# Kernel optimization log

Hardware: AMD Instinct MI355X
Metric: run time of the kernel (lower is better)

Reference implementation:

```python
import jax, jax.numpy as jnp
import numpy as np

EPS = 1e-08  # matches torch default eps in both F.normalize and PairwiseDistance


def setup_inputs() -> dict:
    key = jax.random.key(0)
    x = jax.random.normal(key, (8192, 1024), dtype=jnp.float32)
    return {"x": x}


def reference(x) -> jnp.ndarray:
    B = x.shape[0]
    # F.normalize(x, p=2, dim=-1, eps=EPS): x / max(||x||_2, eps)
    norms = jnp.linalg.norm(x, axis=-1, keepdims=True)
    xn = x / jnp.maximum(norms, EPS)
    # cosine similarity matrix [B, B]
    cos_sim = xn @ xn.T
    # fill_diagonal_(-2): exclude self from nearest-neighbor search
    idx = jnp.arange(B)
    cos_sim = cos_sim.at[idx, idx].set(-2.0)
    nn_idx = jnp.argmax(cos_sim, axis=1)  # [B] int
    # torch PairwiseDistance(p=2, eps=EPS): ||x1 - x2 + eps||_2
    diff = xn - xn[nn_idx] + EPS
    nn_dist = jnp.sqrt(jnp.sum(diff * diff, axis=-1))  # [B]
    loss = -jnp.mean(jnp.log(nn_dist + EPS))
    return loss
```

## Files before the change

kernel.cpp:

```cpp
#include <hip/hip_runtime.h>
#include <hip/hip_bf16.h>
#include <math.h>

#define NB 8192
#define ND 1024
#define KEPS 1e-8f
#define SLOTS 128
#define NTILE 32
#define NWG 528
#define NKT 16

typedef __attribute__((ext_vector_type(8))) __bf16 bf16x8;
typedef __attribute__((ext_vector_type(4))) float f32x4;

__device__ __forceinline__ unsigned int fmono(float f) {
    unsigned int b = __float_as_uint(f);
    return b ^ ((b & 0x80000000u) ? 0xFFFFFFFFu : 0x80000000u);
}
__device__ __forceinline__ unsigned short f2bf(float f) {
    union { float f; unsigned int u; } a;
    a.f = f;
    unsigned int lsb = (a.u >> 16) & 1u;
    a.u += 0x7fffu + lsb;
    return (unsigned short)(a.u >> 16);
}
__device__ __forceinline__ void gload_lds16(const void* g, void* l) {
    __builtin_amdgcn_global_load_lds(
        (const __attribute__((address_space(1))) unsigned int*)g,
        (__attribute__((address_space(3))) unsigned int*)l, 16, 0, 0);
}
__device__ __forceinline__ unsigned long long packmax(float mx, int mc) {
    return ((unsigned long long)fmono(mx) << 32) |
           (unsigned long long)(~(unsigned int)mc);
}

__global__ __launch_bounds__(256) void normalize_k(const float* __restrict__ x,
                                                   unsigned short* __restrict__ xnb) {
    int row = blockIdx.x * 4 + (threadIdx.x >> 6);
    int l = threadIdx.x & 63;
    const float4* xr = (const float4*)(x + (size_t)row * ND);
    float4 v[4];
    float ss = 0.f;
#pragma unroll
    for (int q = 0; q < 4; ++q) {
        v[q] = xr[q * 64 + l];
        ss += v[q].x * v[q].x + v[q].y * v[q].y + v[q].z * v[q].z + v[q].w * v[q].w;
    }
#pragma unroll
    for (int off = 1; off < 64; off <<= 1) ss += __shfl_xor(ss, off, 64);
    float scale = 1.0f / fmaxf(sqrtf(ss), KEPS);
    ushort4* o = (ushort4*)(xnb + (size_t)row * ND);
#pragma unroll
    for (int q = 0; q < 4; ++q) {
        ushort4 u;
        u.x = f2bf(v[q].x * scale);
        u.y = f2bf(v[q].y * scale);
        u.z = f2bf(v[q].z * scale);
        u.w = f2bf(v[q].w * scale);
        o[q * 64 + l] = u;
    }
}

#define FENCE_BARRIER() do { asm volatile("" ::: "memory"); \
    __builtin_amdgcn_s_barrier(); asm volatile("" ::: "memory"); } while (0)
#define LGKM0() do { asm volatile("s_waitcnt lgkmcnt(0)" ::: "memory"); \
    __builtin_amdgcn_sched_barrier(0); } while (0)
#define WAIT_VM6() asm volatile("s_waitcnt vmcnt(6)" ::: "memory")
#define WAIT_VM0() asm volatile("s_waitcnt vmcnt(0)" ::: "memory")

#define STAGE(H, DB) do { \
    gload_lds16(sp[H][0], ldsb + (DB) + (H) * 16384 + wv * 1024); \
    gload_lds16(sp[H][1], ldsb + (DB) + (H) * 16384 + 8192 + wv * 1024); \
    sp[H][0] += 128; sp[H][1] += 128; } while (0)

#define LOAD_A(CB, MQ) do { \
    const char* Ab_ = ldsb + (CB) + ((MQ) * 2 + wM) * 8192 + rowOff; \
    _Pragma("unroll") for (int mi = 0; mi < 4; ++mi) { \
        af[mi][0] = *(const bf16x8*)(Ab_ + mi * 2048 + ks0); \
        af[mi][1] = *(const bf16x8*)(Ab_ + mi * 2048 + ks1); } } while (0)

#define LOAD_B(CB, BANK, NQ) do { \
    const char* Bb_ = ldsb + (CB) + 32768 + (NQ) * 16384 + wN * 4096 + rowOff; \
    _Pragma("unroll") for (int ni = 0; ni < 2; ++ni) { \
        BANK[ni][0] = *(const bf16x8*)(Bb_ + ni * 2048 + ks0); \
        BANK[ni][1] = *(const bf16x8*)(Bb_ + ni * 2048 + ks1); } } while (0)

#define MFMAQ(MH, NH, BANK) do { \
    __builtin_amdgcn_s_setprio(1); \
    _Pragma("unroll") for (int mi = 0; mi < 4; ++mi) \
    _Pragma("unroll") for (int ni = 0; ni < 2; ++ni) { \
        acc[(MH) * 4 + mi][(NH) * 2 + ni] = __builtin_amdgcn_mfma_f32_16x16x32_bf16( \
            af[mi][0], BANK[ni][0], acc[(MH) * 4 + mi][(NH) * 2 + ni], 0, 0, 0); \
        acc[(MH) * 4 + mi][(NH) * 2 + ni] = __builtin_amdgcn_mfma_f32_16x16x32_bf16( \
            af[mi][1], BANK[ni][1], acc[(MH) * 4 + mi][(NH) * 2 + ni], 0, 0, 0); } \
    __builtin_amdgcn_s_setprio(0); } while (0)

#define KTILE(CB, DB, S1, S2, FINAL) do { \
    bf16x8 af[4][2], b0[2][2], b1[2][2]; \
    LOAD_A(CB, 0); LOAD_B(CB, b0, 0); \
    if (S1) STAGE(1, DB); \
    FENCE_BARRIER(); LGKM0(); MFMAQ(0, 0, b0); FENCE_BARRIER(); \
    LOAD_B(CB, b1, 1); \
    if (S2) STAGE(0, CB); \
    FENCE_BARRIER(); LGKM0(); MFMAQ(0, 1, b1); FENCE_BARRIER(); \
    LOAD_A(CB, 1); \
    if (S2) STAGE(2, CB); \
    FENCE_BARRIER(); LGKM0(); MFMAQ(1, 1, b1); FENCE_BARRIER(); \
    if (S2) STAGE(3, CB); \
    FENCE_BARRIER(); MFMAQ(1, 0, b0); \
    if (FINAL) { WAIT_VM0(); } else { WAIT_VM6(); } \
    FENCE_BARRIER(); } while (0)

#define KTILE_LAST(CB) do { \
    bf16x8 af[4][2], b0[2][2], b1[2][2]; \
    LOAD_A(CB, 0); LOAD_B(CB, b0, 0); \
    FENCE_BARRIER(); LGKM0(); MFMAQ(0, 0, b0); FENCE_BARRIER(); \
    LOAD_B(CB, b1, 1); \
    FENCE_BARRIER(); LGKM0(); MFMAQ(0, 1, b1); FENCE_BARRIER(); \
    LOAD_A(CB, 1); \
    FENCE_BARRIER(); LGKM0(); MFMAQ(1, 1, b1); FENCE_BARRIER(); \
    MFMAQ(1, 0, b0); } while (0)

__global__ __launch_bounds__(512, 2) void argmax_gemm(const unsigned short* __restrict__ xnb,
                                                      unsigned long long* __restrict__ partial) {
    extern __shared__ char ldsb[];

    int wg = (int)blockIdx.x;
    int tile = (wg & 7) * (NWG / 8) + (wg >> 3);
    int by = 0, tr = tile;
    while (tr >= NTILE - by) { tr -= NTILE - by; ++by; }
    const int bx = by + tr;

    const int rowBase = by * 256, colBase = bx * 256;
    const int tid = (int)threadIdx.x;
    const int wv = tid >> 6;
    const int l = tid & 63;
    const int wM = wv >> 2;
    const int wN = wv & 3;

    const int rowOff = (l & 15) * 128;
    const int ks0 = (((l >> 4) * 16)) ^ ((l & 7) << 4);
    const int ks1 = (64 | ((l >> 4) * 16)) ^ ((l & 7) << 4);

    const int scol = (((l & 7) ^ (l >> 3)) << 4);
    const char* xb = (const char*)xnb;
    const char* sp[4][2];
#pragma unroll
    for (int q = 0; q < 2; ++q) {
        int R = (q * 8 + wv) * 8 + (l >> 3);
        int arow = (R >> 6) * 128 + (R & 63);
        int bcol = (R >> 5) * 64 + (R & 31);
        sp[0][q] = xb + (size_t)(rowBase + arow) * 2048 + scol;
        sp[1][q] = xb + (size_t)(rowBase + arow + 64) * 2048 + scol;
        sp[2][q] = xb + (size_t)(colBase + bcol) * 2048 + scol;
        sp[3][q] = xb + (size_t)(colBase + bcol + 32) * 2048 + scol;
    }

    f32x4 acc[8][4];
#pragma unroll
    for (int m = 0; m < 8; ++m)
#pragma unroll
        for (int n = 0; n < 4; ++n) acc[m][n] = f32x4{0.f, 0.f, 0.f, 0.f};

    STAGE(0, 0); STAGE(2, 0); STAGE(3, 0); STAGE(1, 0);
    STAGE(0, 65536); STAGE(2, 65536); STAGE(3, 65536);
    WAIT_VM6();
    FENCE_BARRIER();

    for (int c = 0; c < 12; c += 2) {
        KTILE(0, 65536, true, true, false);
        KTILE(65536, 0, true, true, false);
    }
    KTILE(0, 65536, true, true, false);
    KTILE(65536, 0, true, true, false);
    KTILE(0, 65536, true, false, true);
    KTILE_LAST(65536);

#pragma unroll
    for (int m = 0; m < 8; ++m) {
#pragma unroll
        for (int r = 0; r < 4; ++r) {
            int gi = rowBase + wM * 128 + m * 16 + (l >> 4) * 4 + r;
            float mx = -3.0f;
            int mc = 0x7FFFFFFF;
#pragma unroll
            for (int n = 0; n < 4; ++n) {
                int gj = colBase + wN * 64 + n * 16 + (l & 15);
                float v = (gi == gj) ? -2.0f : acc[m][n][r];
                if (v > mx) { mx = v; mc = gj; }
            }
#pragma unroll
            for (int off = 1; off < 16; off <<= 1) {
                float omx = __shfl_xor(mx, off, 64);
                int omc = __shfl_xor(mc, off, 64);
                if (omx > mx || (omx == mx && omc < mc)) { mx = omx; mc = omc; }
            }
            if ((l & 15) == 0)
                partial[(size_t)gi * SLOTS + (2 * by + (bx - by) * 4 + wN)] = packmax(mx, mc);
        }
    }
    if (bx > by) {
#pragma unroll
        for (int n = 0; n < 4; ++n) {
            int gj = colBase + wN * 64 + n * 16 + (l & 15);
            float mx = -3.0f;
            int mc = 0x7FFFFFFF;
#pragma unroll
            for (int m = 0; m < 8; ++m) {
#pragma unroll
                for (int r = 0; r < 4; ++r) {
                    int gi = rowBase + wM * 128 + m * 16 + (l >> 4) * 4 + r;
                    float v = (gi == gj) ? -2.0f : acc[m][n][r];
                    if (v > mx) { mx = v; mc = gi; }
                }
            }
#pragma unroll
            for (int off = 16; off < 64; off <<= 1) {
                float omx = __shfl_xor(mx, off, 64);
                int omc = __shfl_xor(mc, off, 64);
                if (omx > mx || (omx == mx && omc < mc)) { mx = omx; mc = omc; }
            }
            if ((l >> 4) == 0)
                partial[(size_t)gj * SLOTS + (2 * by + wM)] = packmax(mx, mc);
        }
    }
}

__global__ __launch_bounds__(256) void dist_k(const float* __restrict__ x,
                                              const unsigned long long* __restrict__ partial,
                                              float* __restrict__ rowloss) {
    int i = blockIdx.x * 4 + (threadIdx.x >> 6);
    int l = threadIdx.x & 63;
    int nv = SLOTS - 2 * (i >> 8);
    unsigned long long p = 0ull;
    if (l < nv) p = partial[(size_t)i * SLOTS + l];
    if (l + 64 < nv) {
        unsigned long long o = partial[(size_t)i * SLOTS + l + 64];
        if (o > p) p = o;
    }
#pragma unroll
    for (int off = 1; off < 64; off <<= 1) {
        unsigned long long o = __shfl_xor(p, off, 64);
        if (o > p) p = o;
    }
    int j = (int)(~(unsigned int)(p & 0xFFFFFFFFull));

    const float4* xi = (const float4*)(x + (size_t)i * ND);
    const float4* xj = (const float4*)(x + (size_t)j * ND);
    float4 a[4], b[4];
    float sa = 0.f, sb = 0.f;
#pragma unroll
    for (int q = 0; q < 4; ++q) {
        a[q] = xi[q * 64 + l];
        b[q] = xj[q * 64 + l];
        sa += a[q].x * a[q].x + a[q].y * a[q].y + a[q].z * a[q].z + a[q].w * a[q].w;
        sb += b[q].x * b[q].x + b[q].y * b[q].y + b[q].z * b[q].z + b[q].w * b[q].w;
    }
#pragma unroll
    for (int off = 1; off < 64; off <<= 1) {
        sa += __shfl_xor(sa, off, 64);
        sb += __shfl_xor(sb, off, 64);
    }
    float ia = 1.0f / fmaxf(sqrtf(sa), KEPS);
    float ib = 1.0f / fmaxf(sqrtf(sb), KEPS);
    float ss = 0.f;
#pragma unroll
    for (int q = 0; q < 4; ++q) {
        float dx = a[q].x * ia - b[q].x * ib + KEPS;
        float dy = a[q].y * ia - b[q].y * ib + KEPS;
        float dz = a[q].z * ia - b[q].z * ib + KEPS;
        float dw = a[q].w * ia - b[q].w * ib + KEPS;
        ss += dx * dx + dy * dy + dz * dz + dw * dw;
    }
#pragma unroll
    for (int off = 1; off < 64; off <<= 1) ss += __shfl_xor(ss, off, 64);
    if (l == 0) rowloss[i] = -logf(sqrtf(ss) + KEPS);
}

__global__ __launch_bounds__(1024) void reduce_k(const float* __restrict__ rowloss,
                                                 float* __restrict__ out) {
    int t = threadIdx.x;
    float s = 0.0f;
#pragma unroll
    for (int k = 0; k < 8; ++k) s += rowloss[t + k * 1024];
#pragma unroll
    for (int off = 32; off > 0; off >>= 1) s += __shfl_down(s, off, 64);
    __shared__ float sred[16];
    if ((t & 63) == 0) sred[t >> 6] = s;
    __syncthreads();
    if (t == 0) {
        float tot = 0.0f;
        for (int k = 0; k < 16; ++k) tot += sred[k];
        out[0] = tot / (float)NB;
    }
}

extern "C" void kernel_launch(void* const* d_in, const int* in_sizes, int n_in,
                              void* d_out, int out_size, void* d_ws, size_t ws_size,
                              hipStream_t stream) {
    const float* x = (const float*)d_in[0];
    float* out = (float*)d_out;

    char* ws = (char*)d_ws;
    unsigned short* xnb = (unsigned short*)ws;
    unsigned long long* partial =
        (unsigned long long*)(ws + (size_t)NB * ND * 2);
    float* rowloss = (float*)(ws + (size_t)NB * ND * 2 + (size_t)NB * SLOTS * 8);

    (void)hipFuncSetAttribute((const void*)argmax_gemm,
                              hipFuncAttributeMaxDynamicSharedMemorySize, 131072);

    normalize_k<<<NB / 4, 256, 0, stream>>>(x, xnb);
    argmax_gemm<<<NWG, 512, 131072, stream>>>(xnb, partial);
    dist_k<<<NB / 4, 256, 0, stream>>>(x, partial, rowloss);
    reduce_k<<<1, 1024, 0, stream>>>(rowloss, out);
}
```

Measured before the change: 217.6 us.

## Simplify GEMM K-loop to whole-tile prefetch and fuse final reduction into dist kernel

Replaces the interleaved, fine-grained staging schedule in the GEMM main loop with a simple double-buffer. Each k-tile now issues all four global-to-LDS stages for the next buffer up front, then waits and runs all MFMAs, without intermediate barriers, lgkm waits or setprio. Separately, the reduce kernel is removed: the last dist_k block, found via an atomic counter reset in normalize_k, sums the row losses, saving one launch. The simpler schedule may lose the overlap that the fine-grained interleaving gave.

```diff
diff --git a/kernel.cpp b/kernel.cpp
--- a/kernel.cpp
+++ b/kernel.cpp
@@ -9,6 +9,7 @@
 #define NTILE 32
 #define NWG 528
 #define NKT 16
+#define NDBLK (NB / 4)
 
 typedef __attribute__((ext_vector_type(8))) __bf16 bf16x8;
 typedef __attribute__((ext_vector_type(4))) float f32x4;
@@ -35,7 +36,9 @@
 }
 
 __global__ __launch_bounds__(256) void normalize_k(const float* __restrict__ x,
-                                                   unsigned short* __restrict__ xnb) {
+                                                   unsigned short* __restrict__ xnb,
+                                                   unsigned int* __restrict__ counter) {
+    if (blockIdx.x == 0 && threadIdx.x == 0) counter[0] = 0u;
     int row = blockIdx.x * 4 + (threadIdx.x >> 6);
     int l = threadIdx.x & 63;
     const float4* xr = (const float4*)(x + (size_t)row * ND);
@@ -63,9 +66,7 @@
 
 #define FENCE_BARRIER() do { asm volatile("" ::: "memory"); \
     __builtin_amdgcn_s_barrier(); asm volatile("" ::: "memory"); } while (0)
-#define LGKM0() do { asm volatile("s_waitcnt lgkmcnt(0)" ::: "memory"); \
-    __builtin_amdgcn_sched_barrier(0); } while (0)
-#define WAIT_VM6() asm volatile("s_waitcnt vmcnt(6)" ::: "memory")
+#define WAIT_VM8() asm volatile("s_waitcnt vmcnt(8)" ::: "memory")
 #define WAIT_VM0() asm volatile("s_waitcnt vmcnt(0)" ::: "memory")
 
 #define STAGE(H, DB) do { \
@@ -86,40 +87,23 @@
         BANK[ni][1] = *(const bf16x8*)(Bb_ + ni * 2048 + ks1); } } while (0)
 
 #define MFMAQ(MH, NH, BANK) do { \
-    __builtin_amdgcn_s_setprio(1); \
     _Pragma("unroll") for (int mi = 0; mi < 4; ++mi) \
     _Pragma("unroll") for (int ni = 0; ni < 2; ++ni) { \
         acc[(MH) * 4 + mi][(NH) * 2 + ni] = __builtin_amdgcn_mfma_f32_16x16x32_bf16( \
             af[mi][0], BANK[ni][0], acc[(MH) * 4 + mi][(NH) * 2 + ni], 0, 0, 0); \
         acc[(MH) * 4 + mi][(NH) * 2 + ni] = __builtin_amdgcn_mfma_f32_16x16x32_bf16( \
             af[mi][1], BANK[ni][1], acc[(MH) * 4 + mi][(NH) * 2 + ni], 0, 0, 0); } \
-    __builtin_amdgcn_s_setprio(0); } while (0)
-
-#define KTILE(CB, DB, S1, S2, FINAL) do { \
+    } while (0)
+
+#define KT(CB, DB, PF) do { \
+    if (PF) { STAGE(0, DB); STAGE(1, DB); STAGE(2, DB); STAGE(3, DB); WAIT_VM8(); } \
+    else { WAIT_VM0(); } \
+    FENCE_BARRIER(); \
     bf16x8 af[4][2], b0[2][2], b1[2][2]; \
-    LOAD_A(CB, 0); LOAD_B(CB, b0, 0); \
-    if (S1) STAGE(1, DB); \
-    FENCE_BARRIER(); LGKM0(); MFMAQ(0, 0, b0); FENCE_BARRIER(); \
-    LOAD_B(CB, b1, 1); \
-    if (S2) STAGE(0, CB); \
-    FENCE_BARRIER(); LGKM0(); MFMAQ(0, 1, b1); FENCE_BARRIER(); \
-    LOAD_A(CB, 1); \
-    if (S2) STAGE(2, CB); \
-    FENCE_BARRIER(); LGKM0(); MFMAQ(1, 1, b1); FENCE_BARRIER(); \
-    if (S2) STAGE(3, CB); \
-    FENCE_BARRIER(); MFMAQ(1, 0, b0); \
-    if (FINAL) { WAIT_VM0(); } else { WAIT_VM6(); } \
+    LOAD_A(CB, 0); LOAD_B(CB, b0, 0); MFMAQ(0, 0, b0); \
+    LOAD_B(CB, b1, 1); MFMAQ(0, 1, b1); \
+    LOAD_A(CB, 1); MFMAQ(1, 1, b1); MFMAQ(1, 0, b0); \
     FENCE_BARRIER(); } while (0)
-
-#define KTILE_LAST(CB) do { \
-    bf16x8 af[4][2], b0[2][2], b1[2][2]; \
-    LOAD_A(CB, 0); LOAD_B(CB, b0, 0); \
-    FENCE_BARRIER(); LGKM0(); MFMAQ(0, 0, b0); FENCE_BARRIER(); \
-    LOAD_B(CB, b1, 1); \
-    FENCE_BARRIER(); LGKM0(); MFMAQ(0, 1, b1); FENCE_BARRIER(); \
-    LOAD_A(CB, 1); \
-    FENCE_BARRIER(); LGKM0(); MFMAQ(1, 1, b1); FENCE_BARRIER(); \
-    MFMAQ(1, 0, b0); } while (0)
 
 __global__ __launch_bounds__(512, 2) void argmax_gemm(const unsigned short* __restrict__ xnb,
                                                       unsigned long long* __restrict__ partial) {
@@ -156,25 +140,18 @@
         sp[3][q] = xb + (size_t)(colBase + bcol + 32) * 2048 + scol;
     }
 
+    STAGE(0, 0); STAGE(1, 0); STAGE(2, 0); STAGE(3, 0);
+
     f32x4 acc[8][4];
 #pragma unroll
     for (int m = 0; m < 8; ++m)
 #pragma unroll
         for (int n = 0; n < 4; ++n) acc[m][n] = f32x4{0.f, 0.f, 0.f, 0.f};
 
-    STAGE(0, 0); STAGE(2, 0); STAGE(3, 0); STAGE(1, 0);
-    STAGE(0, 65536); STAGE(2, 65536); STAGE(3, 65536);
-    WAIT_VM6();
-    FENCE_BARRIER();
-
-    for (int c = 0; c < 12; c += 2) {
-        KTILE(0, 65536, true, true, false);
-        KTILE(65536, 0, true, true, false);
-    }
-    KTILE(0, 65536, true, true, false);
-    KTILE(65536, 0, true, true, false);
-    KTILE(0, 65536, true, false, true);
-    KTILE_LAST(65536);
+    for (int c = 0; c < NKT; c += 2) {
+        KT(0, 65536, c + 1 < NKT);
+        KT(65536, 0, c + 2 < NKT);
+    }
 
 #pragma unroll
     for (int m = 0; m < 8; ++m) {
@@ -228,7 +205,9 @@
 
 __global__ __launch_bounds__(256) void dist_k(const float* __restrict__ x,
                                               const unsigned long long* __restrict__ partial,
-                                              float* __restrict__ rowloss) {
+                                              float* __restrict__ rowloss,
+                                              unsigned int* __restrict__ counter,
+                                              float* __restrict__ out) {
     int i = blockIdx.x * 4 + (threadIdx.x >> 6);
     int l = threadIdx.x & 63;
     int nv = SLOTS - 2 * (i >> 8);
@@ -274,24 +253,29 @@
     }
 #pragma unroll
     for (int off = 1; off < 64; off <<= 1) ss += __shfl_xor(ss, off, 64);
-    if (l == 0) rowloss[i] = -logf(sqrtf(ss) + KEPS);
-}
-
-__global__ __launch_bounds__(1024) void reduce_k(const float* __restrict__ rowloss,
-                                                 float* __restrict__ out) {
-    int t = threadIdx.x;
-    float s = 0.0f;
-#pragma unroll
-    for (int k = 0; k < 8; ++k) s += rowloss[t + k * 1024];
-#pragma unroll
-    for (int off = 32; off > 0; off >>= 1) s += __shfl_down(s, off, 64);
-    __shared__ float sred[16];
-    if ((t & 63) == 0) sred[t >> 6] = s;
+    if (l == 0) rowloss[i] = logf(sqrtf(ss) + KEPS);
+
+    __shared__ int done_s;
     __syncthreads();
-    if (t == 0) {
-        float tot = 0.0f;
-        for (int k = 0; k < 16; ++k) tot += sred[k];
-        out[0] = tot / (float)NB;
+    if (threadIdx.x == 0) {
+        __threadfence();
+        unsigned int old = atomicAdd(counter, 1u);
+        done_s = (old == (unsigned int)(NDBLK - 1)) ? 1 : 0;
+    }
+    __syncthreads();
+    if (done_s) {
+        __threadfence();
+        int t = threadIdx.x;
+        float s = 0.f;
+#pragma unroll
+        for (int k = 0; k < 32; ++k) s += rowloss[t * 32 + k];
+#pragma unroll
+        for (int off = 1; off < 64; off <<= 1) s += __shfl_xor(s, off, 64);
+        __shared__ float fred[4];
+        if ((t & 63) == 0) fred[t >> 6] = s;
+        __syncthreads();
+        if (t == 0)
+            out[0] = -(fred[0] + fred[1] + fred[2] + fred[3]) / (float)NB;
     }
 }
 
@@ -306,12 +290,12 @@
     unsigned long long* partial =
         (unsigned long long*)(ws + (size_t)NB * ND * 2);
     float* rowloss = (float*)(ws + (size_t)NB * ND * 2 + (size_t)NB * SLOTS * 8);
+    unsigned int* counter = (unsigned int*)(rowloss + NB);
 
     (void)hipFuncSetAttribute((const void*)argmax_gemm,
                               hipFuncAttributeMaxDynamicSharedMemorySize, 131072);
 
-    normalize_k<<<NB / 4, 256, 0, stream>>>(x, xnb);
+    normalize_k<<<NB / 4, 256, 0, stream>>>(x, xnb, counter);
     argmax_gemm<<<NWG, 512, 131072, stream>>>(xnb, partial);
-    dist_k<<<NB / 4, 256, 0, stream>>>(x, partial, rowloss);
-    reduce_k<<<1, 1024, 0, stream>>>(rowloss, out);
-}
+    dist_k<<<NDBLK, 256, 0, stream>>>(x, partial, rowloss, counter, out);
+}
```

Measured after the change: 264.2 us. 21.4% more time.
